# Kernel tuning notes

Hardware: AMD Instinct MI355X
Metric: run time of the kernel (lower is better)

## Reference

```python
import jax, jax.numpy as jnp
import numpy as np

N = 8192          # number of particles
CUTOFF = 0.5      # self.cutoff (final filter uses d_ij <= cutoff)


def setup_inputs() -> dict:
    key = jax.random.key(0)
    k1, _ = jax.random.split(key)
    positions = jax.random.normal(k1, (N, 3), dtype=jnp.float32)
    box_vectors = jnp.eye(3, dtype=jnp.float32)  # orthogonal box, lengths 1.0
    iu, ju = np.triu_indices(N, k=1)             # all unique pairs i < j (as in _init_pairs)
    i_pairs = jnp.asarray(iu, dtype=jnp.int32)
    j_pairs = jnp.asarray(ju, dtype=jnp.int32)
    return {"positions": positions, "box_vectors": box_vectors,
            "i_pairs": i_pairs, "j_pairs": j_pairs, "is_periodic": 1}


def reference(positions, box_vectors, i_pairs, j_pairs, is_periodic):
    # OrthogonalDisplacementFunction: r_ij = x_i - x_j, wrapped into the box
    r_ij = positions[i_pairs] - positions[j_pairs]          # [P, 3]
    if is_periodic:
        box_lengths = jnp.diagonal(box_vectors)             # [3] (orthogonal box)
        half = box_lengths * 0.5
        r_ij = jnp.remainder(r_ij + half, box_lengths) - half
    d_ij = jnp.linalg.norm(r_ij, axis=1, keepdims=True)     # [P, 1]
    # Cutoff filter. torch compacts with boolean indexing (data-dependent shape);
    # for a jit-compatible fixed-shape reference we return a validity mask and
    # zero the entries of filtered-out pairs (only_unique_pairs=True branch).
    mask = d_ij[:, 0] <= CUTOFF                              # [P]
    pair_indices = jnp.stack([i_pairs, j_pairs])             # [2, P]
    r_out = jnp.where(mask[:, None], r_ij, 0.0)
    d_out = jnp.where(mask[:, None], d_ij, 0.0)
    return pair_indices, d_out, r_out, mask
```

## Files before the change

kernel.cpp:

```cpp
#include <hip/hip_runtime.h>
#include <math.h>


__device__ __forceinline__ float bf2f(unsigned short h) {
    return __uint_as_float(((unsigned)h) << 16);
}

__device__ __forceinline__ float rem_np(float x, float L) {
    float fm = fmodf(x, L);
    if (fm != 0.0f && ((fm < 0.0f) != (L < 0.0f))) fm += L;
    return fm;
}

__device__ __forceinline__ float rem1_np(float x) {
    float fm = __fsub_rn(x, truncf(x));
    if (fm < 0.0f) fm = __fadd_rn(fm, 1.0f);
    return fm;
}

template <bool F32>
__device__ __forceinline__ void load_pos(const void* __restrict__ pos, int idx,
                                         float& x, float& y, float& z) {
    if (F32) {
        const float* q = (const float*)pos + 3 * idx;
        x = q[0]; y = q[1]; z = q[2];
    } else {
        const unsigned short* q = (const unsigned short*)pos + 3 * idx;
        x = bf2f(q[0]); y = bf2f(q[1]); z = bf2f(q[2]);
    }
}

template <bool F32>
__device__ __forceinline__ void body(const void* __restrict__ pos,
                                     float Lx, float Ly, float Lz,
                                     bool periodic, bool unit, int N, long long P,
                                     int i, int j, long long t,
                                     float* __restrict__ out) {
    const float hx = __fmul_rn(Lx, 0.5f);
    const float hy = __fmul_rn(Ly, 0.5f);
    const float hz = __fmul_rn(Lz, 0.5f);

    float fi[4], fj[4], fd[4], fm[4], fr[12];

    float xi, yi, zi;
    load_pos<F32>(pos, i, xi, yi, zi);

#pragma unroll
    for (int k = 0; k < 4; ++k) {
        float xj, yj, zj;
        load_pos<F32>(pos, j, xj, yj, zj);
        float rx = __fsub_rn(xi, xj);
        float ry = __fsub_rn(yi, yj);
        float rz = __fsub_rn(zi, zj);
        if (periodic) {
            float vx = __fadd_rn(rx, hx);
            float vy = __fadd_rn(ry, hy);
            float vz = __fadd_rn(rz, hz);
            if (unit) {
                rx = __fsub_rn(rem1_np(vx), hx);
                ry = __fsub_rn(rem1_np(vy), hy);
                rz = __fsub_rn(rem1_np(vz), hz);
            } else {
                rx = __fsub_rn(rem_np(vx, Lx), hx);
                ry = __fsub_rn(rem_np(vy, Ly), hy);
                rz = __fsub_rn(rem_np(vz, Lz), hz);
            }
        }
        float d2 = __fadd_rn(__fadd_rn(__fmul_rn(rx, rx), __fmul_rn(ry, ry)),
                             __fmul_rn(rz, rz));
        float d = sqrtf(d2);
        bool m = (d <= 0.5f);

        fi[k] = (float)i;
        fj[k] = (float)j;
        fd[k] = m ? d : 0.0f;
        fm[k] = m ? 1.0f : 0.0f;
        fr[3 * k + 0] = m ? rx : 0.0f;
        fr[3 * k + 1] = m ? ry : 0.0f;
        fr[3 * k + 2] = m ? rz : 0.0f;

        if (k < 3) {
            ++j;
            if (j >= N) {
                ++i;
                j = i + 1;
                load_pos<F32>(pos, i, xi, yi, zi);
            }
        }
    }

    ((float4*)(out))[t]          = make_float4(fi[0], fi[1], fi[2], fi[3]);
    ((float4*)(out + P))[t]      = make_float4(fj[0], fj[1], fj[2], fj[3]);
    ((float4*)(out + 2 * P))[t]  = make_float4(fd[0], fd[1], fd[2], fd[3]);
    float4* orr = (float4*)(out + 3 * P);
    orr[3 * t + 0] = make_float4(fr[0], fr[1], fr[2], fr[3]);
    orr[3 * t + 1] = make_float4(fr[4], fr[5], fr[6], fr[7]);
    orr[3 * t + 2] = make_float4(fr[8], fr[9], fr[10], fr[11]);
    ((float4*)(out + 6 * P))[t]  = make_float4(fm[0], fm[1], fm[2], fm[3]);
}

__global__ __launch_bounds__(256) void nsq_kernel(const void* __restrict__ pos,
                                                  const unsigned* __restrict__ box_raw,
                                                  const int* __restrict__ isper,
                                                  float* __restrict__ out,
                                                  int N, long long P) {
    long long t = (long long)blockIdx.x * blockDim.x + threadIdx.x;
    long long p0 = t << 2;
    if (p0 >= P) return;

    const bool f32 = (box_raw[0] == 0x3F800000u);

    float Lx, Ly, Lz;
    if (f32) {
        const float* b = (const float*)box_raw;
        Lx = b[0]; Ly = b[4]; Lz = b[8];
    } else {
        const unsigned short* b = (const unsigned short*)box_raw;
        Lx = bf2f(b[0]); Ly = bf2f(b[4]); Lz = bf2f(b[8]);
    }
    const bool periodic = (isper[0] != 0);
    const bool unit = (Lx == 1.0f) && (Ly == 1.0f) && (Lz == 1.0f);

    const double M = 2.0 * (double)N - 1.0;
    int i = (int)((M - sqrt(M * M - 8.0 * (double)p0)) * 0.5);
    if (i < 0) i = 0;
    if (i > N - 2) i = N - 2;
    auto off = [N](long long a) { return a * (2LL * N - 1 - a) / 2; };
    while (i < N - 2 && off(i + 1) <= p0) ++i;
    while (i > 0 && off(i) > p0) --i;
    int j = (int)((long long)i + 1 + (p0 - off(i)));

    if (f32)
        body<true>(pos, Lx, Ly, Lz, periodic, unit, N, P, i, j, t, out);
    else
        body<false>(pos, Lx, Ly, Lz, periodic, unit, N, P, i, j, t, out);
}

extern "C" void kernel_launch(void* const* d_in, const int* in_sizes, int n_in,
                              void* d_out, int out_size, void* d_ws, size_t ws_size,
                              hipStream_t stream) {
    const void* pos = d_in[0];
    const unsigned* box = (const unsigned*)d_in[1];
    const int* isper = (const int*)d_in[4];

    long long P = (long long)out_size / 7;
    int N = in_sizes[0] / 3;

    long long nthreads = (P + 3) >> 2;
    int blocks = (int)((nthreads + 255) / 256);
    nsq_kernel<<<blocks, 256, 0, stream>>>(pos, box, isper, (float*)d_out, N, P);
}
```

Baseline: 1.026 ms.

## Stage r_ij output through LDS for coalesced stores; use float sqrt for row index

Each wavefront now writes its three float4 r_ij values into a per-wave LDS buffer, then reads them back transposed so that global stores from adjacent lanes are contiguous and coalesced. Before, each lane wrote three consecutive float4s, so the lanes' stores were strided. The initial row estimate also switches from double-precision sqrt to a float sqrt, which is cheaper on the GPU. The existing correction loops fix the estimate, though float error for large D may make them run extra iterations. The LDS path relies on wavefront-synchronous execution, with only a waitcnt and no barrier.

New measurement: 1.022 ms. No clear change (-0.4%).

```diff
diff --git a/kernel.cpp b/kernel.cpp
--- a/kernel.cpp
+++ b/kernel.cpp
@@ -35,7 +35,8 @@
                                      float Lx, float Ly, float Lz,
                                      bool periodic, bool unit, int N, long long P,
                                      int i, int j, long long t,
-                                     float* __restrict__ out) {
+                                     float* __restrict__ out,
+                                     float4* __restrict__ smw, bool fullwave) {
     const float hx = __fmul_rn(Lx, 0.5f);
     const float hy = __fmul_rn(Ly, 0.5f);
     const float hz = __fmul_rn(Lz, 0.5f);
@@ -89,14 +90,34 @@
         }
     }
 
-    ((float4*)(out))[t]          = make_float4(fi[0], fi[1], fi[2], fi[3]);
-    ((float4*)(out + P))[t]      = make_float4(fj[0], fj[1], fj[2], fj[3]);
-    ((float4*)(out + 2 * P))[t]  = make_float4(fd[0], fd[1], fd[2], fd[3]);
-    float4* orr = (float4*)(out + 3 * P);
-    orr[3 * t + 0] = make_float4(fr[0], fr[1], fr[2], fr[3]);
-    orr[3 * t + 1] = make_float4(fr[4], fr[5], fr[6], fr[7]);
-    orr[3 * t + 2] = make_float4(fr[8], fr[9], fr[10], fr[11]);
-    ((float4*)(out + 6 * P))[t]  = make_float4(fm[0], fm[1], fm[2], fm[3]);
+    ((float4*)(out))[t]         = make_float4(fi[0], fi[1], fi[2], fi[3]);
+    ((float4*)(out + P))[t]     = make_float4(fj[0], fj[1], fj[2], fj[3]);
+    ((float4*)(out + 2 * P))[t] = make_float4(fd[0], fd[1], fd[2], fd[3]);
+    ((float4*)(out + 6 * P))[t] = make_float4(fm[0], fm[1], fm[2], fm[3]);
+
+    const float4 r0 = make_float4(fr[0], fr[1], fr[2], fr[3]);
+    const float4 r1 = make_float4(fr[4], fr[5], fr[6], fr[7]);
+    const float4 r2 = make_float4(fr[8], fr[9], fr[10], fr[11]);
+
+    if (fullwave) {
+        const int lane = (int)(t & 63);
+        smw[3 * lane + 0] = r0;
+        smw[3 * lane + 1] = r1;
+        smw[3 * lane + 2] = r2;
+        asm volatile("s_waitcnt lgkmcnt(0)" ::: "memory");
+        float4 a = smw[lane];
+        float4 b = smw[64 + lane];
+        float4 c = smw[128 + lane];
+        float4* g = (float4*)(out + 3 * P) + (t >> 6) * 192;
+        g[lane]       = a;
+        g[64 + lane]  = b;
+        g[128 + lane] = c;
+    } else {
+        float4* orr = (float4*)(out + 3 * P);
+        orr[3 * t + 0] = r0;
+        orr[3 * t + 1] = r1;
+        orr[3 * t + 2] = r2;
+    }
 }
 
 __global__ __launch_bounds__(256) void nsq_kernel(const void* __restrict__ pos,
@@ -104,6 +125,8 @@
                                                   const int* __restrict__ isper,
                                                   float* __restrict__ out,
                                                   int N, long long P) {
+    __shared__ float4 sm[4][192];
+
     long long t = (long long)blockIdx.x * blockDim.x + threadIdx.x;
     long long p0 = t << 2;
     if (p0 >= P) return;
@@ -121,8 +144,9 @@
     const bool periodic = (isper[0] != 0);
     const bool unit = (Lx == 1.0f) && (Ly == 1.0f) && (Lz == 1.0f);
 
-    const double M = 2.0 * (double)N - 1.0;
-    int i = (int)((M - sqrt(M * M - 8.0 * (double)p0)) * 0.5);
+    const long long M = 2LL * N - 1;
+    const long long D = M * M - 8 * p0;
+    int i = (int)(((float)M - __fsqrt_rn((float)D)) * 0.5f);
     if (i < 0) i = 0;
     if (i > N - 2) i = N - 2;
     auto off = [N](long long a) { return a * (2LL * N - 1 - a) / 2; };
@@ -130,10 +154,13 @@
     while (i > 0 && off(i) > p0) --i;
     int j = (int)((long long)i + 1 + (p0 - off(i)));
 
+    const bool fullwave = ((((t | 63) << 2) | 3) < P);
+    float4* smw = &sm[threadIdx.x >> 6][0];
+
     if (f32)
-        body<true>(pos, Lx, Ly, Lz, periodic, unit, N, P, i, j, t, out);
+        body<true>(pos, Lx, Ly, Lz, periodic, unit, N, P, i, j, t, out, smw, fullwave);
     else
-        body<false>(pos, Lx, Ly, Lz, periodic, unit, N, P, i, j, t, out);
+        body<false>(pos, Lx, Ly, Lz, periodic, unit, N, P, i, j, t, out, smw, fullwave);
 }
 
 extern "C" void kernel_launch(void* const* d_in, const int* in_sizes, int n_in,
```
